# Kernel optimization log

Measured on AMD Instinct MI355X. Metric: run time of the kernel, lower is better.

The kernel has to match this reference:

```python
import jax, jax.numpy as jnp
import numpy as np

B, S, HID, NH, HD, NL = 2, 4096, 1024, 16, 64, 128
N_ITER = 6


def setup_inputs() -> dict:
    key = jax.random.key(0)
    ks = jax.random.split(key, 9)
    s = 0.02
    D = NH * HD
    return {
        "X": jax.random.normal(ks[0], (B, S, HID), jnp.float32),
        "mask": jnp.ones((B, S), jnp.float32),
        "Wq": jax.random.normal(ks[1], (HID, D), jnp.float32) * s,
        "bq": jnp.zeros((D,), jnp.float32),
        "Wk": jax.random.normal(ks[2], (HID, D), jnp.float32) * s,
        "bk": jnp.zeros((D,), jnp.float32),
        "Wv": jax.random.normal(ks[3], (HID, D), jnp.float32) * s,
        "bv": jnp.zeros((D,), jnp.float32),
        "Wo": jax.random.normal(ks[4], (D, HID), jnp.float32) * s,
        "bo": jnp.zeros((HID,), jnp.float32),
    }


def iterative_inv(mat, n_iter=N_ITER):
    # Newton-Schulz style pseudo-inverse iteration (Nystromformer 'original' init)
    I = jnp.eye(mat.shape[-1], dtype=mat.dtype)
    K = mat
    V = K.swapaxes(-1, -2) / jnp.max(jnp.sum(K, axis=-2))
    for _ in range(n_iter):
        KV = K @ V
        V = 0.25 * V @ (13.0 * I - KV @ (15.0 * I - KV @ (7.0 * I - KV)))
    return V


def nystrom_core(Q, K, V, mask):
    # Q,K,V: [B,NH,S,HD], mask: [B,S]
    scale = 1.0 / np.sqrt(np.sqrt(HD))  # 1/d^(1/4) applied to both Q and K
    m = mask[:, None, :, None]
    Q = Q * m * scale
    K = K * m * scale
    seg = S // NL
    # landmarks: mean over contiguous segments -> [B,NH,NL,HD]
    Ql = Q.reshape(B, NH, NL, seg, HD).mean(axis=-2)
    Kl = K.reshape(B, NH, NL, seg, HD).mean(axis=-2)
    k1 = jax.nn.softmax(jnp.einsum('bhsd,bhld->bhsl', Q, Kl), axis=-1)   # [B,NH,S,NL]
    k2 = jax.nn.softmax(jnp.einsum('bhld,bhmd->bhlm', Ql, Kl), axis=-1)  # [B,NH,NL,NL]
    k3 = jax.nn.softmax(
        jnp.einsum('bhld,bhsd->bhls', Ql, K) - 1e9 * (1.0 - mask[:, None, None, :]),
        axis=-1)                                                          # [B,NH,NL,S]
    return k1 @ iterative_inv(k2) @ (k3 @ V)                              # [B,NH,S,HD]


def reference(X, mask, Wq, bq, Wk, bk, Wv, bv, Wo, bo):
    def split(Y):  # [B,S,NH*HD] -> [B,NH,S,HD]
        return Y.reshape(B, S, NH, HD).transpose(0, 2, 1, 3)
    Q = split(X @ Wq + bq)
    K = split(X @ Wk + bk)
    V = split(X @ Wv + bv)
    attn = nystrom_core(Q.astype(jnp.float32), K.astype(jnp.float32),
                        V.astype(jnp.float32), mask.astype(jnp.float32))
    out = attn.transpose(0, 2, 1, 3).reshape(B, S, NH * HD)
    return out @ Wo + bo
```

## Files before the change

kernel.cpp:

```cpp
#include <hip/hip_runtime.h>
#include <math.h>

constexpr int cB = 2, cS = 4096, cHID = 1024, cNH = 16, cHD = 64, cNL = 128, cSEG = 32, cD = 1024, cBH = 32;
constexpr float cSCALE = 0.35355339059327373f;

typedef _Float16 f16x8 __attribute__((ext_vector_type(8)));
typedef float f32x4 __attribute__((ext_vector_type(4)));

__device__ inline void gload_lds16(const void* g, void* l) {
    __builtin_amdgcn_global_load_lds(
        (const __attribute__((address_space(1))) void*)g,
        (__attribute__((address_space(3))) void*)l, 16, 0, 0);
}

__global__ __launch_bounds__(256) void cast_x(const float* __restrict__ X, _Float16* __restrict__ Xh)
{
    int i = (blockIdx.x * 256 + threadIdx.x) * 4;
    float4 v = *reinterpret_cast<const float4*>(X + i);
    union { _Float16 h[4]; ushort4 u; } p;
    p.h[0] = (_Float16)v.x; p.h[1] = (_Float16)v.y; p.h[2] = (_Float16)v.z; p.h[3] = (_Float16)v.w;
    *reinterpret_cast<ushort4*>(Xh + i) = p.u;
}

__global__ __launch_bounds__(256) void wcast_t(
    const float* __restrict__ Wq, const float* __restrict__ Wk,
    const float* __restrict__ Wv, const float* __restrict__ Wo,
    _Float16* __restrict__ WqT, _Float16* __restrict__ WkT,
    _Float16* __restrict__ WvT, _Float16* __restrict__ WoT)
{
    __shared__ float tile[32][33];
    const int wsel = blockIdx.z;
    const float* W = (wsel == 0) ? Wq : (wsel == 1 ? Wk : (wsel == 2 ? Wv : Wo));
    _Float16* WT   = (wsel == 0) ? WqT : (wsel == 1 ? WkT : (wsel == 2 ? WvT : WoT));
    const int n0 = blockIdx.x * 32, k0 = blockIdx.y * 32;
    const int t = threadIdx.x;
    const int r = t >> 3, c = (t & 7) * 4;
    float4 v = *reinterpret_cast<const float4*>(W + (size_t)(k0 + r) * cD + n0 + c);
    tile[r][c] = v.x; tile[r][c + 1] = v.y; tile[r][c + 2] = v.z; tile[r][c + 3] = v.w;
    __syncthreads();
    union { _Float16 h[4]; ushort4 u; } p;
    p.h[0] = (_Float16)tile[c + 0][r]; p.h[1] = (_Float16)tile[c + 1][r];
    p.h[2] = (_Float16)tile[c + 2][r]; p.h[3] = (_Float16)tile[c + 3][r];
    *reinterpret_cast<ushort4*>(WT + (size_t)(n0 + r) * cHID + k0 + c) = p.u;
}

__global__ __launch_bounds__(256) void xm_kernel(
    const float* __restrict__ X, const float* __restrict__ mask,
    float* __restrict__ Xm, float* __restrict__ mbar)
{
    const int bl = blockIdx.x;
    const int b = bl >> 7, l = bl & 127;
    const int c = threadIdx.x * 4;
    float4 a = {0.f, 0.f, 0.f, 0.f};
    float msum = 0.f;
    for (int j = 0; j < cSEG; ++j) {
        float m = mask[b * cS + l * cSEG + j];
        float4 x = *reinterpret_cast<const float4*>(X + ((size_t)(b * cS + l * cSEG + j)) * cHID + c);
        a.x += m * x.x; a.y += m * x.y; a.z += m * x.z; a.w += m * x.w;
        msum += m;
    }
    const float inv = 1.0f / cSEG;
    a.x *= inv; a.y *= inv; a.z *= inv; a.w *= inv;
    *reinterpret_cast<float4*>(Xm + (size_t)bl * cHID + c) = a;
    if (threadIdx.x == 0) mbar[bl] = msum * inv;
}

__global__ __launch_bounds__(256) void qkv_gemm_f16(
    const _Float16* __restrict__ Xh, const float* __restrict__ mask,
    const _Float16* __restrict__ WqT, const _Float16* __restrict__ WkT, const _Float16* __restrict__ WvT,
    const float* __restrict__ bq, const float* __restrict__ bk, const float* __restrict__ bv,
    _Float16* __restrict__ Qh, _Float16* __restrict__ Kh, _Float16* __restrict__ Vh)
{
    __shared__ __align__(16) _Float16 As[128 * 64];
    __shared__ __align__(16) _Float16 Bs[128 * 64];
    const int wsel = blockIdx.z;
    const _Float16* WT = (wsel == 0) ? WqT : (wsel == 1 ? WkT : WvT);
    const float* bias  = (wsel == 0) ? bq  : (wsel == 1 ? bk  : bv);
    _Float16* Y        = (wsel == 0) ? Qh  : (wsel == 1 ? Kh  : Vh);
    const int n0 = blockIdx.x * 128, m0 = blockIdx.y * 128;
    const int t = threadIdx.x;
    const int wave = t >> 6, lane = t & 63;
    const int wm = (wave >> 1) * 64, wn = (wave & 1) * 64;
    const int quad = lane >> 4, l15 = lane & 15;
    const int srow = wave * 8 + (lane >> 3);
    const int scol = (lane & 7) * 8;

    f32x4 acc[4][4];
#pragma unroll
    for (int i = 0; i < 4; ++i)
#pragma unroll
        for (int j = 0; j < 4; ++j) acc[i][j] = (f32x4){0.f, 0.f, 0.f, 0.f};

    for (int k0 = 0; k0 < cHID; k0 += 64) {
        const _Float16* aSrc = Xh + (size_t)(m0 + srow) * cHID + k0 + scol;
        const _Float16* bSrc = WT + (size_t)(n0 + srow) * cHID + k0 + scol;
#pragma unroll
        for (int i = 0; i < 4; ++i) {
            gload_lds16(aSrc + (size_t)(i * 32) * cHID, &As[(wave * 8 + i * 32) * 64]);
            gload_lds16(bSrc + (size_t)(i * 32) * cHID, &Bs[(wave * 8 + i * 32) * 64]);
        }
        __syncthreads();
        f16x8 af[2][4], bf[2][4];
#pragma unroll
        for (int kh = 0; kh < 2; ++kh) {
#pragma unroll
            for (int mt = 0; mt < 4; ++mt)
                af[kh][mt] = *reinterpret_cast<const f16x8*>(&As[(wm + mt * 16 + l15) * 64 + kh * 32 + quad * 8]);
#pragma unroll
            for (int nt = 0; nt < 4; ++nt)
                bf[kh][nt] = *reinterpret_cast<const f16x8*>(&Bs[(wn + nt * 16 + l15) * 64 + kh * 32 + quad * 8]);
        }
#pragma unroll
        for (int kh = 0; kh < 2; ++kh)
#pragma unroll
            for (int mt = 0; mt < 4; ++mt)
#pragma unroll
                for (int nt = 0; nt < 4; ++nt)
                    acc[mt][nt] = __builtin_amdgcn_mfma_f32_16x16x32_f16(af[kh][mt], bf[kh][nt], acc[mt][nt], 0, 0, 0);
        __syncthreads();
    }
#pragma unroll
    for (int mt = 0; mt < 4; ++mt) {
#pragma unroll
        for (int r = 0; r < 4; ++r) {
            int R = m0 + wm + mt * 16 + quad * 4 + r;
            int b = R >> 12, s = R & (cS - 1);
            float msc = (wsel < 2) ? mask[b * cS + s] * cSCALE : 1.0f;
#pragma unroll
            for (int nt = 0; nt < 4; ++nt) {
                int Cc = n0 + wn + nt * 16 + l15;
                int h = Cc >> 6, d = Cc & 63;
                float val = (acc[mt][nt][r] + bias[Cc]) * msc;
                Y[((size_t)(b * cNH + h) * cS + s) * cHD + d] = (_Float16)val;
            }
        }
    }
}

__global__ __launch_bounds__(256) void out_gemm_f16(
    const _Float16* __restrict__ Ah, const _Float16* __restrict__ WT,
    const float* __restrict__ bias, float* __restrict__ Y)
{
    __shared__ __align__(16) _Float16 As[128 * 64];
    __shared__ __align__(16) _Float16 Bs[128 * 64];
    const int n0 = blockIdx.x * 128, m0 = blockIdx.y * 128;
    const int t = threadIdx.x;
    const int wave = t >> 6, lane = t & 63;
    const int wm = (wave >> 1) * 64, wn = (wave & 1) * 64;
    const int quad = lane >> 4, l15 = lane & 15;
    const int srow = wave * 8 + (lane >> 3);
    const int scol = (lane & 7) * 8;

    f32x4 acc[4][4];
#pragma unroll
    for (int i = 0; i < 4; ++i)
#pragma unroll
        for (int j = 0; j < 4; ++j) acc[i][j] = (f32x4){0.f, 0.f, 0.f, 0.f};

    for (int k0 = 0; k0 < cD; k0 += 64) {
        const _Float16* aSrc = Ah + (size_t)(m0 + srow) * cD + k0 + scol;
        const _Float16* bSrc = WT + (size_t)(n0 + srow) * cD + k0 + scol;
#pragma unroll
        for (int i = 0; i < 4; ++i) {
            gload_lds16(aSrc + (size_t)(i * 32) * cD, &As[(wave * 8 + i * 32) * 64]);
            gload_lds16(bSrc + (size_t)(i * 32) * cD, &Bs[(wave * 8 + i * 32) * 64]);
        }
        __syncthreads();
        f16x8 af[2][4], bf[2][4];
#pragma unroll
        for (int kh = 0; kh < 2; ++kh) {
#pragma unroll
            for (int mt = 0; mt < 4; ++mt)
                af[kh][mt] = *reinterpret_cast<const f16x8*>(&As[(wm + mt * 16 + l15) * 64 + kh * 32 + quad * 8]);
#pragma unroll
            for (int nt = 0; nt < 4; ++nt)
                bf[kh][nt] = *reinterpret_cast<const f16x8*>(&Bs[(wn + nt * 16 + l15) * 64 + kh * 32 + quad * 8]);
        }
#pragma unroll
        for (int kh = 0; kh < 2; ++kh)
#pragma unroll
            for (int mt = 0; mt < 4; ++mt)
#pragma unroll
                for (int nt = 0; nt < 4; ++nt)
                    acc[mt][nt] = __builtin_amdgcn_mfma_f32_16x16x32_f16(af[kh][mt], bf[kh][nt], acc[mt][nt], 0, 0, 0);
        __syncthreads();
    }
#pragma unroll
    for (int mt = 0; mt < 4; ++mt) {
#pragma unroll
        for (int r = 0; r < 4; ++r) {
            int R = m0 + wm + mt * 16 + quad * 4 + r;
#pragma unroll
            for (int nt = 0; nt < 4; ++nt) {
                int Cc = n0 + wn + nt * 16 + l15;
                Y[(size_t)R * cHID + Cc] = acc[mt][nt][r] + bias[Cc];
            }
        }
    }
}

__global__ __launch_bounds__(256) void lgemm(
    const float* __restrict__ Xm, const float* __restrict__ mbar,
    const float* __restrict__ Wq, const float* __restrict__ bq,
    const float* __restrict__ Wk, const float* __restrict__ bk,
    float* __restrict__ Ql, float* __restrict__ Kl,
    _Float16* __restrict__ Qlh, _Float16* __restrict__ Klh)
{
    __shared__ __align__(16) float As[16][68];
    __shared__ __align__(16) float Bs[16][68];
    const int tid = threadIdx.x;
    const int wsel = blockIdx.z;
    const float* W    = wsel ? Wk : Wq;
    const float* bias = wsel ? bk : bq;
    float* Yl         = wsel ? Kl : Ql;
    _Float16* Ylh     = wsel ? Klh : Qlh;
    const int c0 = blockIdx.x * 64, r0 = blockIdx.y * 64;
    const int tx = tid & 15, ty = tid >> 4;
    const int am = tid >> 2, ak = (tid & 3) * 4;
    const int bkk = tid >> 4, bn = (tid & 15) * 4;

    float acc[4][4] = {};
    for (int k0 = 0; k0 < cHID; k0 += 16) {
        float4 a4 = *reinterpret_cast<const float4*>(Xm + (size_t)(r0 + am) * cHID + k0 + ak);
        As[ak + 0][am] = a4.x; As[ak + 1][am] = a4.y; As[ak + 2][am] = a4.z; As[ak + 3][am] = a4.w;
        float4 b4 = *reinterpret_cast<const float4*>(W + (size_t)(k0 + bkk) * cD + c0 + bn);
        *reinterpret_cast<float4*>(&Bs[bkk][bn]) = b4;
        __syncthreads();
#pragma unroll
        for (int kk = 0; kk < 16; ++kk) {
            float4 av  = *reinterpret_cast<const float4*>(&As[kk][ty * 4]);
            float4 bv4 = *reinterpret_cast<const float4*>(&Bs[kk][tx * 4]);
            float a_[4] = {av.x, av.y, av.z, av.w};
            float b_[4] = {bv4.x, bv4.y, bv4.z, bv4.w};
#pragma unroll
            for (int i = 0; i < 4; ++i)
#pragma unroll
                for (int j = 0; j < 4; ++j) acc[i][j] += a_[i] * b_[j];
        }
        __syncthreads();
    }
#pragma unroll
    for (int i = 0; i < 4; ++i) {
        int r = r0 + ty * 4 + i;
        int b = r >> 7, l = r & 127;
        float mb = mbar[r];
#pragma unroll
        for (int j = 0; j < 4; ++j) {
            int c = c0 + tx * 4 + j;
            int h = c >> 6, d = c & 63;
            float val = (acc[i][j] + mb * bias[c]) * cSCALE;
            size_t idx = ((size_t)(b * cNH + h) * cNL + l) * cHD + d;
            Yl[idx] = val;
            Ylh[idx] = (_Float16)val;
        }
    }
}

__global__ __launch_bounds__(128) void k2_softmax(
    const float* __restrict__ Ql, const float* __restrict__ Kl, float* __restrict__ k2)
{
    __shared__ __align__(16) float qrow[64];
    __shared__ float red[128];
    int bh = blockIdx.x >> 7, i = blockIdx.x & 127;
    int j = threadIdx.x;
    if (j < 64) qrow[j] = Ql[(bh * cNL + i) * cHD + j];
    __syncthreads();
    const float4* q4  = reinterpret_cast<const float4*>(qrow);
    const float4* kl4 = reinterpret_cast<const float4*>(Kl + (bh * cNL + j) * cHD);
    float dot = 0.f;
#pragma unroll
    for (int u = 0; u < 16; ++u) {
        float4 a = q4[u], b = kl4[u];
        dot += a.x * b.x + a.y * b.y + a.z * b.z + a.w * b.w;
    }
    red[j] = dot; __syncthreads();
    for (int off = 64; off > 0; off >>= 1) { if (j < off) red[j] = fmaxf(red[j], red[j + off]); __syncthreads(); }
    float m = red[0]; __syncthreads();
    float e = expf(dot - m);
    red[j] = e; __syncthreads();
    for (int off = 64; off > 0; off >>= 1) { if (j < off) red[j] += red[j + off]; __syncthreads(); }
    k2[(bh * cNL + i) * cNL + j] = e / red[0];
}

__global__ __launch_bounds__(128) void colsum_max(const float* __restrict__ k2, int* __restrict__ cmax)
{
    __shared__ float red[128];
    int bh = blockIdx.x, j = threadIdx.x;
    float s = 0.f;
    for (int i = 0; i < cNL; ++i) s += k2[(bh * cNL + i) * cNL + j];
    red[j] = s; __syncthreads();
    for (int off = 64; off > 0; off >>= 1) { if (j < off) red[j] = fmaxf(red[j], red[j + off]); __syncthreads(); }
    if (j == 0) atomicMax(cmax, __float_as_int(red[0]));
}

__device__ inline void split2(float v, _Float16& h, _Float16& l) {
    h = (_Float16)v;
    l = (_Float16)(v - (float)h);
}

#define NYS_MFMA(a, b, c) __builtin_amdgcn_mfma_f32_16x16x32_f16((a), (b), (c), 0, 0, 0)

#define NYS_PRODUCT(PH, PL, LH, LL)                                                     \
    {                                                                                   \
        _Pragma("unroll")                                                               \
        for (int nt_ = 0; nt_ < 8; ++nt_) {                                             \
            f32x4 a0_ = (f32x4){0.f, 0.f, 0.f, 0.f};                                    \
            f32x4 a1_ = (f32x4){0.f, 0.f, 0.f, 0.f};                                    \
            _Pragma("unroll")                                                           \
            for (int k0_ = 0; k0_ < 4; ++k0_) {                                         \
                f16x8 bh_ = *reinterpret_cast<const f16x8*>(&PH[(nt_ * 16 + l15) * 136 + k0_ * 32 + quad * 8]); \
                f16x8 bl_ = *reinterpret_cast<const f16x8*>(&PL[(nt_ * 16 + l15) * 136 + k0_ * 32 + quad * 8]); \
                a0_ = NYS_MFMA(LH[0][k0_], bh_, a0_);                                   \
                a1_ = NYS_MFMA(LH[1][k0_], bh_, a1_);                                   \
                a0_ = NYS_MFMA(LL[0][k0_], bh_, a0_);                                   \
                a1_ = NYS_MFMA(LL[1][k0_], bh_, a1_);                                   \
                a0_ = NYS_MFMA(LH[0][k0_], bl_, a0_);                                   \
                a1_ = NYS_MFMA(LH[1][k0_], bl_, a1_);                                   \
            }                                                                           \
            acc[0][nt_] = a0_; acc[1][nt_] = a1_;                                       \
        }                                                                               \
    }

#define NYS_SCATTER_W(alphav)                                                           \
    {                                                                                   \
        _Pragma("unroll")                                                               \
        for (int mt_ = 0; mt_ < 2; ++mt_) {                                             \
            _Pragma("unroll")                                                           \
            for (int nt_ = 0; nt_ < 8; ++nt_) {                                         \
                int col_ = nt_ * 16 + l15;                                              \
                int rb_  = wave * 32 + mt_ * 16 + quad * 4;                             \
                ushort4 ph_, pl_;                                                       \
                _Pragma("unroll")                                                       \
                for (int r_ = 0; r_ < 4; ++r_) {                                        \
                    float v_ = ((rb_ + r_) == col_ ? (alphav) : 0.f) - acc[mt_][nt_][r_]; \
                    _Float16 h_, l_; split2(v_, h_, l_);                                \
                    ((unsigned short*)&ph_)[r_] = __builtin_bit_cast(unsigned short, h_); \
                    ((unsigned short*)&pl_)[r_] = __builtin_bit_cast(unsigned short, l_); \
                }                                                                       \
                *reinterpret_cast<ushort4*>(&Whi_s[col_ * 136 + rb_]) = ph_;            \
                *reinterpret_cast<ushort4*>(&Wlo_s[col_ * 136 + rb_]) = pl_;            \
            }                                                                           \
        }                                                                               \
    }

__global__ __launch_bounds__(256, 1) void nys_fused(
    const float* __restrict__ k2, const int* __restrict__ cmax, float* __restrict__ V6)
{
    __shared__ __align__(16) _Float16 Vhi_s[128 * 136];
    __shared__ __align__(16) _Float16 Vlo_s[128 * 136];
    __shared__ __align__(16) _Float16 Whi_s[128 * 136];
    __shared__ __align__(16) _Float16 Wlo_s[128 * 136];
    const int bh = blockIdx.x;
    const int t = threadIdx.x;
    const int wave = t >> 6, lane = t & 63;
    const int quad = lane >> 4, l15 = lane & 15;
    const float* Kg = k2 + (size_t)bh * (cNL * cNL);
    const float invc = 1.0f / __int_as_float(*cmax);

#pragma unroll
    for (int i = 0; i < 16; ++i) {
        int idx = t + i * 256;
        int row = idx >> 5, c4 = (idx & 31) * 4;
        float4 v = *reinterpret_cast<const float4*>(Kg + (size_t)row * cNL + c4);
        ushort4 ph, pl;
        _Float16 h, l;
        split2(v.x * invc, h, l); ((unsigned short*)&ph)[0] = __builtin_bit_cast(unsigned short, h); ((unsigned short*)&pl)[0] = __builtin_bit_cast(unsigned short, l);
        split2(v.y * invc, h, l); ((unsigned short*)&ph)[1] = __builtin_bit_cast(unsigned short, h); ((unsigned short*)&pl)[1] = __builtin_bit_cast(unsigned short, l);
        split2(v.z * invc, h, l); ((unsigned short*)&ph)[2] = __builtin_bit_cast(unsigned short, h); ((unsigned short*)&pl)[2] = __builtin_bit_cast(unsigned short, l);
        split2(v.w * invc, h, l); ((unsigned short*)&ph)[3] = __builtin_bit_cast(unsigned short, h); ((unsigned short*)&pl)[3] = __builtin_bit_cast(unsigned short, l);
        *reinterpret_cast<ushort4*>(&Vhi_s[row * 136 + c4]) = ph;
        *reinterpret_cast<ushort4*>(&Vlo_s[row * 136 + c4]) = pl;
    }

    f16x8 Khi[2][4], Klo[2][4];
#pragma unroll
    for (int mt = 0; mt < 2; ++mt) {
        const int rowL = wave * 32 + mt * 16 + l15;
#pragma unroll
        for (int k0 = 0; k0 < 4; ++k0) {
            const float* src = Kg + (size_t)rowL * cNL + k0 * 32 + quad * 8;
            union { f16x8 v; _Float16 e[8]; } hh, ll;
#pragma unroll
            for (int j = 0; j < 8; ++j) split2(src[j], hh.e[j], ll.e[j]);
            Khi[mt][k0] = hh.v; Klo[mt][k0] = ll.v;
        }
    }
    __syncthreads();

    f32x4 acc[2][8];
    f16x8 Ahi[2][4], Alo[2][4];

    for (int it = 0; it < 6; ++it) {
        NYS_PRODUCT(Vhi_s, Vlo_s, Khi, Klo);
        NYS_SCATTER_W(7.0f);
        __syncthreads();

#pragma unroll
        for (int mt = 0; mt < 2; ++mt) {
            const int rowL = wave * 32 + mt * 16 + l15;
#pragma unroll
            for (int k0 = 0; k0 < 4; ++k0) {
                union { f16x8 v; _Float16 e[8]; } hh, ll;
#pragma unroll
                for (int j = 0; j < 8; ++j) {
                    int kk = k0 * 32 + quad * 8 + j;
                    float s = (float)Whi_s[kk * 136 + rowL] + (float)Wlo_s[kk * 136 + rowL];
                    float a = ((kk == rowL) ? 7.0f : 0.0f) - s;
                    split2(a, hh.e[j], ll.e[j]);
                }
                Ahi[mt][k0] = hh.v; Alo[mt][k0] = ll.v;
            }
        }

        NYS_PRODUCT(Whi_s, Wlo_s, Ahi, Alo);
        __syncthreads();
        NYS_SCATTER_W(15.0f);
        __syncthreads();

        NYS_PRODUCT(Whi_s, Wlo_s, Ahi, Alo);

        f16x8 Vlh[2][4], Vll[2][4];
#pragma unroll
        for (int mt = 0; mt < 2; ++mt) {
            const int rowL = wave * 32 + mt * 16 + l15;
#pragma unroll
            for (int k0 = 0; k0 < 4; ++k0) {
                union { f16x8 v; _Float16 e[8]; } hh, ll;
#pragma unroll
                for (int j = 0; j < 8; ++j) {
                    int kk = k0 * 32 + quad * 8 + j;
                    hh.e[j] = Vhi_s[kk * 136 + rowL];
                    ll.e[j] = Vlo_s[kk * 136 + rowL];
                }
                Vlh[mt][k0] = hh.v; Vll[mt][k0] = ll.v;
            }
        }
        __syncthreads();
        NYS_SCATTER_W(13.0f);
        __syncthreads();

        NYS_PRODUCT(Whi_s, Wlo_s, Vlh, Vll);
        if (it < 5) {
#pragma unroll
            for (int mt = 0; mt < 2; ++mt) {
#pragma unroll
                for (int nt = 0; nt < 8; ++nt) {
                    int col = nt * 16 + l15;
                    int rb  = wave * 32 + mt * 16 + quad * 4;
                    ushort4 ph, pl;
#pragma unroll
                    for (int r = 0; r < 4; ++r) {
                        _Float16 h, l; split2(0.25f * acc[mt][nt][r], h, l);
                        ((unsigned short*)&ph)[r] = __builtin_bit_cast(unsigned short, h);
                        ((unsigned short*)&pl)[r] = __builtin_bit_cast(unsigned short, l);
                    }
                    *reinterpret_cast<ushort4*>(&Vhi_s[col * 136 + rb]) = ph;
                    *reinterpret_cast<ushort4*>(&Vlo_s[col * 136 + rb]) = pl;
                }
            }
            __syncthreads();
        }
    }
#pragma unroll
    for (int mt = 0; mt < 2; ++mt)
#pragma unroll
        for (int nt = 0; nt < 8; ++nt)
#pragma unroll
            for (int r = 0; r < 4; ++r) {
                int row = wave * 32 + mt * 16 + quad * 4 + r;
                int col = nt * 16 + l15;
                V6[(size_t)bh * (cNL * cNL) + row * cNL + col] = 0.25f * acc[mt][nt][r];
            }
}

__global__ __launch_bounds__(256) void vtrans(const _Float16* __restrict__ Vh, _Float16* __restrict__ VTh)
{
    __shared__ ushort T[64][72];
    const int s0 = blockIdx.x * 64, bh = blockIdx.y;
    const int t = threadIdx.x;
    const _Float16* vb = Vh + ((size_t)bh * cS + s0) * cHD;
#pragma unroll
    for (int i = 0; i < 2; ++i) {
        int idx = t + i * 256;
        int row = idx >> 3, c8 = idx & 7;
        f16x8 v = *reinterpret_cast<const f16x8*>(vb + (size_t)row * cHD + c8 * 8);
#pragma unroll
        for (int j = 0; j < 8; ++j) T[row][c8 * 8 + j] = ((ushort*)&v)[j];
    }
    __syncthreads();
    _Float16* vt = VTh + (size_t)bh * cHD * cS;
#pragma unroll
    for (int i = 0; i < 2; ++i) {
        int idx = t + i * 256;
        int d = idx >> 3, s8 = idx & 7;
        f16x8 o;
#pragma unroll
        for (int j = 0; j < 8; ++j) ((ushort*)&o)[j] = T[s8 * 8 + j][d];
        *reinterpret_cast<f16x8*>(vt + (size_t)d * cS + s0 + s8 * 8) = o;
    }
}

__global__ __launch_bounds__(256) void k3v_mfma(
    const _Float16* __restrict__ Qlh, const _Float16* __restrict__ Kh,
    const _Float16* __restrict__ VTh, const float* __restrict__ mask,
    float* __restrict__ Opart, float* __restrict__ mpart, float* __restrict__ spart)
{
    __shared__ __align__(16) _Float16 Ps[128 * 72];
    __shared__ float msk[256];
    const int z = blockIdx.x, bh = blockIdx.y;
    const int b = bh >> 4;
    const int sbase = z * 256;
    const int t = threadIdx.x;
    const int wave = t >> 6, lane = t & 63;
    const int quad = lane >> 4, l15 = lane & 15;

    msk[t] = mask[b * cS + sbase + t];

    f16x8 aq[2][2];
    const _Float16* qlg = Qlh + (size_t)bh * cNL * cHD;
#pragma unroll
    for (int mt = 0; mt < 2; ++mt)
#pragma unroll
        for (int k0 = 0; k0 < 2; ++k0)
            aq[mt][k0] = *reinterpret_cast<const f16x8*>(
                qlg + (size_t)(wave * 32 + mt * 16 + l15) * cHD + k0 * 32 + quad * 8);

    float mrun[2][4], srun[2][4];
    f32x4 accO[2][4];
#pragma unroll
    for (int mt = 0; mt < 2; ++mt)
#pragma unroll
        for (int r = 0; r < 4; ++r) { mrun[mt][r] = -1e30f; srun[mt][r] = 0.f; }
#pragma unroll
    for (int mt = 0; mt < 2; ++mt)
#pragma unroll
        for (int dt = 0; dt < 4; ++dt) accO[mt][dt] = (f32x4){0.f, 0.f, 0.f, 0.f};

    __syncthreads();

    const _Float16* kg = Kh + (size_t)bh * cS * cHD;
    const _Float16* vg = VTh + (size_t)bh * cHD * cS;

    for (int step = 0; step < 4; ++step) {
        const int st = sbase + step * 64;
        f32x4 accS[2][4];
#pragma unroll
        for (int mt = 0; mt < 2; ++mt)
#pragma unroll
            for (int nt = 0; nt < 4; ++nt) accS[mt][nt] = (f32x4){0.f, 0.f, 0.f, 0.f};
#pragma unroll
        for (int k0 = 0; k0 < 2; ++k0)
#pragma unroll
            for (int nt = 0; nt < 4; ++nt) {
                f16x8 bk = *reinterpret_cast<const f16x8*>(
                    kg + (size_t)(st + nt * 16 + l15) * cHD + k0 * 32 + quad * 8);
#pragma unroll
                for (int mt = 0; mt < 2; ++mt)
                    accS[mt][nt] = __builtin_amdgcn_mfma_f32_16x16x32_f16(aq[mt][k0], bk, accS[mt][nt], 0, 0, 0);
            }
#pragma unroll
        for (int nt = 0; nt < 4; ++nt) {
            float pen = 1e9f * (1.0f - msk[step * 64 + nt * 16 + l15]);
#pragma unroll
            for (int mt = 0; mt < 2; ++mt)
#pragma unroll
                for (int r = 0; r < 4; ++r) accS[mt][nt][r] -= pen;
        }
#pragma unroll
        for (int mt = 0; mt < 2; ++mt) {
#pragma unroll
            for (int r = 0; r < 4; ++r) {
                float tmax = fmaxf(fmaxf(accS[mt][0][r], accS[mt][1][r]),
                                   fmaxf(accS[mt][2][r], accS[mt][3][r]));
#pragma unroll
                for (int w = 1; w < 16; w <<= 1) tmax = fmaxf(tmax, __shfl_xor(tmax, w, 16));
                float mnew = fmaxf(mrun[mt][r], tmax);
                float alpha = __expf(mrun[mt][r] - mnew);
                float ts = 0.f;
#pragma unroll
                for (int nt = 0; nt < 4; ++nt) {
                    float e = __expf(accS[mt][nt][r] - mnew);
                    accS[mt][nt][r] = e; ts += e;
                }
#pragma unroll
                for (int w = 1; w < 16; w <<= 1) ts += __shfl_xor(ts, w, 16);
                srun[mt][r] = srun[mt][r] * alpha + ts;
                mrun[mt][r] = mnew;
#pragma unroll
                for (int dt = 0; dt < 4; ++dt) accO[mt][dt][r] *= alpha;
            }
        }
#pragma unroll
        for (int mt = 0; mt < 2; ++mt)
#pragma unroll
            for (int nt = 0; nt < 4; ++nt)
#pragma unroll
                for (int r = 0; r < 4; ++r)
                    Ps[(wave * 32 + mt * 16 + quad * 4 + r) * 72 + nt * 16 + l15] =
                        (_Float16)accS[mt][nt][r];
#pragma unroll
        for (int k0 = 0; k0 < 2; ++k0) {
            f16x8 ap[2];
#pragma unroll
            for (int mt = 0; mt < 2; ++mt)
                ap[mt] = *reinterpret_cast<const f16x8*>(
                    &Ps[(wave * 32 + mt * 16 + l15) * 72 + k0 * 32 + quad * 8]);
#pragma unroll
            for (int dt = 0; dt < 4; ++dt) {
                f16x8 bv = *reinterpret_cast<const f16x8*>(
                    vg + (size_t)(dt * 16 + l15) * cS + st + k0 * 32 + quad * 8);
#pragma unroll
                for (int mt = 0; mt < 2; ++mt)
                    accO[mt][dt] = __builtin_amdgcn_mfma_f32_16x16x32_f16(ap[mt], bv, accO[mt][dt], 0, 0, 0);
            }
        }
    }
    const int rowbase = bh * cNL + wave * 32;
#pragma unroll
    for (int mt = 0; mt < 2; ++mt)
#pragma unroll
        for (int dt = 0; dt < 4; ++dt)
#pragma unroll
            for (int r = 0; r < 4; ++r)
                Opart[(size_t)(z * 4096 + rowbase + mt * 16 + quad * 4 + r) * cHD + dt * 16 + l15] =
                    accO[mt][dt][r];
    if (l15 == 0) {
#pragma unroll
        for (int mt = 0; mt < 2; ++mt)
#pragma unroll
            for (int r = 0; r < 4; ++r) {
                int prow = z * 4096 + rowbase + mt * 16 + quad * 4 + r;
                mpart[prow] = mrun[mt][r];
                spart[prow] = srun[mt][r];
            }
    }
}

__global__ __launch_bounds__(256) void k3v_reduce(
    const float* __restrict__ Opart, const float* __restrict__ mpart,
    const float* __restrict__ spart, float* __restrict__ CV)
{
    const int t = threadIdx.x;
    const int row = blockIdx.x * 4 + (t >> 6);
    const int d = t & 63;
    float mstar = -1e30f;
#pragma unroll
    for (int z = 0; z < 16; ++z) mstar = fmaxf(mstar, mpart[z * 4096 + row]);
    float ssum = 0.f, acc = 0.f;
#pragma unroll
    for (int z = 0; z < 16; ++z) {
        float w = __expf(mpart[z * 4096 + row] - mstar);
        ssum += w * spart[z * 4096 + row];
        acc  += w * Opart[(size_t)(z * 4096 + row) * cHD + d];
    }
    CV[(size_t)row * cHD + d] = acc / ssum;
}

__global__ __launch_bounds__(256) void w2_matmul(
    const float* __restrict__ V6, const float* __restrict__ CV, _Float16* __restrict__ W2T)
{
    __shared__ __align__(16) float CVs[128][64];
    const int bh = blockIdx.x, t = threadIdx.x;
    for (int k = 0; k < 32; ++k) { int idx = t + k * 256; CVs[idx >> 6][idx & 63] = CV[bh * 8192 + idx]; }
    __syncthreads();
    const int tx = t & 15, ty = t >> 4;
    float acc[8][4] = {};
    for (int k = 0; k < 128; ++k) {
        float4 b4 = *reinterpret_cast<const float4*>(&CVs[k][tx * 4]);
#pragma unroll
        for (int i = 0; i < 8; ++i) {
            float a = V6[(bh * cNL + ty * 8 + i) * cNL + k];
            acc[i][0] += a * b4.x; acc[i][1] += a * b4.y; acc[i][2] += a * b4.z; acc[i][3] += a * b4.w;
        }
    }
    _Float16* wt = W2T + (size_t)bh * cHD * cNL;
#pragma unroll
    for (int i = 0; i < 8; ++i)
#pragma unroll
        for (int j = 0; j < 4; ++j)
            wt[(size_t)(tx * 4 + j) * cNL + ty * 8 + i] = (_Float16)acc[i][j];
}

__global__ __launch_bounds__(256) void k1_mfma(
    const _Float16* __restrict__ Qh, const _Float16* __restrict__ Klh,
    const _Float16* __restrict__ W2T, _Float16* __restrict__ ctxh)
{
    __shared__ __align__(16) _Float16 Qs[64 * 72];
    __shared__ __align__(16) _Float16 Ps[64 * 136];
    const int s0 = blockIdx.x * 64, bh = blockIdx.y;
    const int b = bh >> 4, h = bh & 15;
    const int t = threadIdx.x;
    const int wave = t >> 6, lane = t & 63;
    const int quad = lane >> 4, l15 = lane & 15;

    {
        const _Float16* qg = Qh + ((size_t)bh * cS + s0) * cHD;
#pragma unroll
        for (int i = 0; i < 2; ++i) {
            int idx = t + i * 256;
            int row = idx >> 3, c8 = idx & 7;
            *reinterpret_cast<f16x8*>(&Qs[row * 72 + c8 * 8]) =
                *reinterpret_cast<const f16x8*>(qg + (size_t)row * cHD + c8 * 8);
        }
    }
    __syncthreads();

    const _Float16* klg = Klh + (size_t)bh * cNL * cHD;
    f32x4 accS[8];
#pragma unroll
    for (int nt = 0; nt < 8; ++nt) accS[nt] = (f32x4){0.f, 0.f, 0.f, 0.f};
#pragma unroll
    for (int k0 = 0; k0 < 2; ++k0) {
        f16x8 aq = *reinterpret_cast<const f16x8*>(&Qs[(wave * 16 + l15) * 72 + k0 * 32 + quad * 8]);
#pragma unroll
        for (int nt = 0; nt < 8; ++nt) {
            f16x8 bk = *reinterpret_cast<const f16x8*>(klg + (size_t)(nt * 16 + l15) * cHD + k0 * 32 + quad * 8);
            accS[nt] = __builtin_amdgcn_mfma_f32_16x16x32_f16(aq, bk, accS[nt], 0, 0, 0);
        }
    }

    float rmax[4] = {-1e30f, -1e30f, -1e30f, -1e30f};
#pragma unroll
    for (int nt = 0; nt < 8; ++nt)
#pragma unroll
        for (int r = 0; r < 4; ++r) rmax[r] = fmaxf(rmax[r], accS[nt][r]);
#pragma unroll
    for (int r = 0; r < 4; ++r)
#pragma unroll
        for (int w = 1; w < 16; w <<= 1) rmax[r] = fmaxf(rmax[r], __shfl_xor(rmax[r], w, 16));
    float rsum[4] = {0.f, 0.f, 0.f, 0.f};
#pragma unroll
    for (int nt = 0; nt < 8; ++nt)
#pragma unroll
        for (int r = 0; r < 4; ++r) { accS[nt][r] = __expf(accS[nt][r] - rmax[r]); rsum[r] += accS[nt][r]; }
#pragma unroll
    for (int r = 0; r < 4; ++r) {
#pragma unroll
        for (int w = 1; w < 16; w <<= 1) rsum[r] += __shfl_xor(rsum[r], w, 16);
        rsum[r] = 1.0f / rsum[r];
    }
#pragma unroll
    for (int nt = 0; nt < 8; ++nt)
#pragma unroll
        for (int r = 0; r < 4; ++r)
            Ps[(wave * 16 + quad * 4 + r) * 136 + nt * 16 + l15] = (_Float16)(accS[nt][r] * rsum[r]);
    __syncthreads();

    const _Float16* wtg = W2T + (size_t)bh * cHD * cNL;
    f32x4 accO[4];
#pragma unroll
    for (int nt = 0; nt < 4; ++nt) accO[nt] = (f32x4){0.f, 0.f, 0.f, 0.f};
#pragma unroll
    for (int k0 = 0; k0 < 4; ++k0) {
        f16x8 ap = *reinterpret_cast<const f16x8*>(&Ps[(wave * 16 + l15) * 136 + k0 * 32 + quad * 8]);
#pragma unroll
        for (int nt = 0; nt < 4; ++nt) {
            f16x8 bw = *reinterpret_cast<const f16x8*>(wtg + (size_t)(nt * 16 + l15) * cNL + k0 * 32 + quad * 8);
            accO[nt] = __builtin_amdgcn_mfma_f32_16x16x32_f16(ap, bw, accO[nt], 0, 0, 0);
        }
    }
#pragma unroll
    for (int nt = 0; nt < 4; ++nt)
#pragma unroll
        for (int r = 0; r < 4; ++r) {
            int s = s0 + wave * 16 + quad * 4 + r;
            int d = nt * 16 + l15;
            ctxh[((size_t)(b * cS) + s) * cD + h * cHD + d] = (_Float16)accO[nt][r];
        }
}

extern "C" void kernel_launch(void* const* d_in, const int* in_sizes, int n_in,
                              void* d_out, int out_size, void* d_ws, size_t ws_size,
                              hipStream_t stream)
{
    const float* X    = (const float*)d_in[0];
    const float* mask = (const float*)d_in[1];
    const float* Wq   = (const float*)d_in[2];
    const float* bq   = (const float*)d_in[3];
    const float* Wk   = (const float*)d_in[4];
    const float* bk   = (const float*)d_in[5];
    const float* Wv   = (const float*)d_in[6];
    const float* bv   = (const float*)d_in[7];
    const float* Wo   = (const float*)d_in[8];
    const float* bo   = (const float*)d_in[9];
    float* out = (float*)d_out;

    float* ws = (float*)d_ws;
    size_t off = 0;
    const size_t szQKV = (size_t)cBH * cS * cHD;
    const size_t szL   = (size_t)cBH * cNL * cHD;
    const size_t szM   = (size_t)cBH * cNL * cNL;
    float* Qr   = ws + off; off += szQKV;
    float* Kr   = ws + off; off += szQKV;
    float* Vr   = ws + off; off += szQKV;
    _Float16* Xh  = (_Float16*)(ws + off); off += szQKV / 2;
    _Float16* WqT = (_Float16*)(ws + off); off += 524288;
    _Float16* WkT = (_Float16*)(ws + off); off += 524288;
    _Float16* WvT = (_Float16*)(ws + off); off += 524288;
    _Float16* WoT = (_Float16*)(ws + off); off += 524288;
    float* Xm   = ws + off; off += (size_t)cB * cNL * cHID;
    float* mbar = ws + off; off += 256;
    float* Ql  = ws + off; off += szL;
    float* Kl  = ws + off; off += szL;
    float* k2  = ws + off; off += szM;
    float* Vb0 = ws + off; off += szM;
    float* Vb1 = ws + off; off += szM;
    float* Zb  = ws + off; off += szM;
    float* T2b = ws + off; off += szM;
    float* T3b = ws + off; off += szM;
    float* CV  = ws + off; off += szL;
    _Float16* Qlh  = (_Float16*)(ws + off); off += szL / 2;
    _Float16* Klh  = (_Float16*)(ws + off); off += szL / 2;
    _Float16* W2Th = (_Float16*)(ws + off); off += szL / 2;
    int*   cmax = (int*)(ws + off); off += 16;
    float* mpart = ws + off; off += 65536;
    float* spart = ws + off; off += 65536;

    _Float16* Qh   = (_Float16*)Qr;
    float*    Opart = Qr + szQKV / 2;
    _Float16* Kh   = (_Float16*)Kr;
    _Float16* ctxh = (_Float16*)(Kr + szQKV / 2);
    _Float16* Vh   = (_Float16*)Vr;
    _Float16* VTh  = (_Float16*)(Vr + szQKV / 2);

    (void)Vb1; (void)Zb; (void)T2b; (void)T3b;

    hipMemsetAsync(cmax, 0, sizeof(int), stream);

    cast_x<<<(int)(szQKV / 1024), 256, 0, stream>>>(X, Xh);
    wcast_t<<<dim3(32, 32, 4), 256, 0, stream>>>(Wq, Wk, Wv, Wo, WqT, WkT, WvT, WoT);
    xm_kernel<<<cB * cNL, 256, 0, stream>>>(X, mask, Xm, mbar);

    qkv_gemm_f16<<<dim3(cD / 128, (cB * cS) / 128, 3), 256, 0, stream>>>(
        Xh, mask, WqT, WkT, WvT, bq, bk, bv, Qh, Kh, Vh);
    vtrans<<<dim3(cS / 64, cBH), 256, 0, stream>>>(Vh, VTh);
    lgemm<<<dim3(cD / 64, (cB * cNL) / 64, 2), 256, 0, stream>>>(Xm, mbar, Wq, bq, Wk, bk, Ql, Kl, Qlh, Klh);

    k2_softmax<<<cBH * cNL, 128, 0, stream>>>(Ql, Kl, k2);
    colsum_max<<<cBH, 128, 0, stream>>>(k2, cmax);

    nys_fused<<<cBH, 256, 0, stream>>>(k2, cmax, Vb0);

    k3v_mfma<<<dim3(16, cBH), 256, 0, stream>>>(Qlh, Kh, VTh, mask, Opart, mpart, spart);
    k3v_reduce<<<1024, 256, 0, stream>>>(Opart, mpart, spart, CV);
    w2_matmul<<<cBH, 256, 0, stream>>>(Vb0, CV, W2Th);
    k1_mfma<<<dim3(cS / 64, cBH), 256, 0, stream>>>(Qh, Klh, W2Th, ctxh);
    out_gemm_f16<<<dim3(cHID / 128, (cB * cS) / 128), 256, 0, stream>>>(ctxh, WoT, bo, out);
}
```

Before: 556.1 us.

## Split Nystrom inverse kernel across 8 waves with 2D wave tiling

The fused Newton-Schulz inverse kernel now runs 512 threads per block instead of 256. Waves are arranged as a 4x2 grid, so each wave computes a 32x64 output tile instead of 32x128, which halves its accumulator registers. The final product now loads the V operand per k-slice instead of staging all of it in registers first, and initial loads use float4. This is meant to add latency hiding to a kernel that runs only 32 blocks, at the cost of an extra barrier per iteration.

```diff
diff --git a/kernel.cpp b/kernel.cpp
--- a/kernel.cpp
+++ b/kernel.cpp
@@ -303,13 +303,14 @@
 #define NYS_PRODUCT(PH, PL, LH, LL)                                                     \
     {                                                                                   \
         _Pragma("unroll")                                                               \
-        for (int nt_ = 0; nt_ < 8; ++nt_) {                                             \
+        for (int nt_ = 0; nt_ < 4; ++nt_) {                                             \
             f32x4 a0_ = (f32x4){0.f, 0.f, 0.f, 0.f};                                    \
             f32x4 a1_ = (f32x4){0.f, 0.f, 0.f, 0.f};                                    \
             _Pragma("unroll")                                                           \
             for (int k0_ = 0; k0_ < 4; ++k0_) {                                         \
-                f16x8 bh_ = *reinterpret_cast<const f16x8*>(&PH[(nt_ * 16 + l15) * 136 + k0_ * 32 + quad * 8]); \
-                f16x8 bl_ = *reinterpret_cast<const f16x8*>(&PL[(nt_ * 16 + l15) * 136 + k0_ * 32 + quad * 8]); \
+                const int boff_ = (wcb + nt_ * 16) * 136 + k0_ * 32 + quad * 8;         \
+                f16x8 bh_ = *reinterpret_cast<const f16x8*>(&PH[boff_]);                \
+                f16x8 bl_ = *reinterpret_cast<const f16x8*>(&PL[boff_]);                \
                 a0_ = NYS_MFMA(LH[0][k0_], bh_, a0_);                                   \
                 a1_ = NYS_MFMA(LH[1][k0_], bh_, a1_);                                   \
                 a0_ = NYS_MFMA(LL[0][k0_], bh_, a0_);                                   \
@@ -326,9 +327,9 @@
         _Pragma("unroll")                                                               \
         for (int mt_ = 0; mt_ < 2; ++mt_) {                                             \
             _Pragma("unroll")                                                           \
-            for (int nt_ = 0; nt_ < 8; ++nt_) {                                         \
-                int col_ = nt_ * 16 + l15;                                              \
-                int rb_  = wave * 32 + mt_ * 16 + quad * 4;                             \
+            for (int nt_ = 0; nt_ < 4; ++nt_) {                                         \
+                int col_ = wcb + nt_ * 16;                                              \
+                int rb_  = wr * 32 + mt_ * 16 + quad * 4;                               \
                 ushort4 ph_, pl_;                                                       \
                 _Pragma("unroll")                                                       \
                 for (int r_ = 0; r_ < 4; ++r_) {                                        \
@@ -343,7 +344,7 @@
         }                                                                               \
     }
 
-__global__ __launch_bounds__(256, 1) void nys_fused(
+__global__ __launch_bounds__(512, 2) void nys_fused(
     const float* __restrict__ k2, const int* __restrict__ cmax, float* __restrict__ V6)
 {
     __shared__ __align__(16) _Float16 Vhi_s[128 * 136];
@@ -353,13 +354,15 @@
     const int bh = blockIdx.x;
     const int t = threadIdx.x;
     const int wave = t >> 6, lane = t & 63;
+    const int wr = wave >> 1, wc = wave & 1;
     const int quad = lane >> 4, l15 = lane & 15;
+    const int wcb = wc * 64 + l15;
     const float* Kg = k2 + (size_t)bh * (cNL * cNL);
     const float invc = 1.0f / __int_as_float(*cmax);
 
 #pragma unroll
-    for (int i = 0; i < 16; ++i) {
-        int idx = t + i * 256;
+    for (int i = 0; i < 8; ++i) {
+        int idx = t + i * 512;
         int row = idx >> 5, c4 = (idx & 31) * 4;
         float4 v = *reinterpret_cast<const float4*>(Kg + (size_t)row * cNL + c4);
         ushort4 ph, pl;
@@ -375,19 +378,23 @@
     f16x8 Khi[2][4], Klo[2][4];
 #pragma unroll
     for (int mt = 0; mt < 2; ++mt) {
-        const int rowL = wave * 32 + mt * 16 + l15;
+        const int rowL = wr * 32 + mt * 16 + l15;
 #pragma unroll
         for (int k0 = 0; k0 < 4; ++k0) {
             const float* src = Kg + (size_t)rowL * cNL + k0 * 32 + quad * 8;
+            float4 v0 = *reinterpret_cast<const float4*>(src);
+            float4 v1 = *reinterpret_cast<const float4*>(src + 4);
             union { f16x8 v; _Float16 e[8]; } hh, ll;
-#pragma unroll
-            for (int j = 0; j < 8; ++j) split2(src[j], hh.e[j], ll.e[j]);
+            split2(v0.x, hh.e[0], ll.e[0]); split2(v0.y, hh.e[1], ll.e[1]);
+            split2(v0.z, hh.e[2], ll.e[2]); split2(v0.w, hh.e[3], ll.e[3]);
+            split2(v1.x, hh.e[4], ll.e[4]); split2(v1.y, hh.e[5], ll.e[5]);
+            split2(v1.z, hh.e[6], ll.e[6]); split2(v1.w, hh.e[7], ll.e[7]);
             Khi[mt][k0] = hh.v; Klo[mt][k0] = ll.v;
         }
     }
     __syncthreads();
 
-    f32x4 acc[2][8];
+    f32x4 acc[2][4];
     f16x8 Ahi[2][4], Alo[2][4];
 
     for (int it = 0; it < 6; ++it) {
@@ -397,7 +404,7 @@
 
 #pragma unroll
         for (int mt = 0; mt < 2; ++mt) {
-            const int rowL = wave * 32 + mt * 16 + l15;
+            const int rowL = wr * 32 + mt * 16 + l15;
 #pragma unroll
             for (int k0 = 0; k0 < 4; ++k0) {
                 union { f16x8 v; _Float16 e[8]; } hh, ll;
@@ -418,13 +425,20 @@
         __syncthreads();
 
         NYS_PRODUCT(Whi_s, Wlo_s, Ahi, Alo);
-
-        f16x8 Vlh[2][4], Vll[2][4];
-#pragma unroll
-        for (int mt = 0; mt < 2; ++mt) {
-            const int rowL = wave * 32 + mt * 16 + l15;
-#pragma unroll
-            for (int k0 = 0; k0 < 4; ++k0) {
+        __syncthreads();
+        NYS_SCATTER_W(13.0f);
+        __syncthreads();
+
+#pragma unroll
+        for (int mt = 0; mt < 2; ++mt)
+#pragma unroll
+            for (int nt = 0; nt < 4; ++nt) acc[mt][nt] = (f32x4){0.f, 0.f, 0.f, 0.f};
+#pragma unroll
+        for (int k0 = 0; k0 < 4; ++k0) {
+            f16x8 Vlh[2], Vll[2];
+#pragma unroll
+            for (int mt = 0; mt < 2; ++mt) {
+                const int rowL = wr * 32 + mt * 16 + l15;
                 union { f16x8 v; _Float16 e[8]; } hh, ll;
 #pragma unroll
                 for (int j = 0; j < 8; ++j) {
@@ -432,21 +446,29 @@
                     hh.e[j] = Vhi_s[kk * 136 + rowL];
                     ll.e[j] = Vlo_s[kk * 136 + rowL];
                 }
-                Vlh[mt][k0] = hh.v; Vll[mt][k0] = ll.v;
-            }
-        }
-        __syncthreads();
-        NYS_SCATTER_W(13.0f);
-        __syncthreads();
-
-        NYS_PRODUCT(Whi_s, Wlo_s, Vlh, Vll);
+                Vlh[mt] = hh.v; Vll[mt] = ll.v;
+            }
+#pragma unroll
+            for (int nt = 0; nt < 4; ++nt) {
+                const int boff = (wcb + nt * 16) * 136 + k0 * 32 + quad * 8;
+                f16x8 bh_ = *reinterpret_cast<const f16x8*>(&Whi_s[boff]);
+                f16x8 bl_ = *reinterpret_cast<const f16x8*>(&Wlo_s[boff]);
+                acc[0][nt] = NYS_MFMA(Vlh[0], bh_, acc[0][nt]);
+                acc[1][nt] = NYS_MFMA(Vlh[1], bh_, acc[1][nt]);
+                acc[0][nt] = NYS_MFMA(Vll[0], bh_, acc[0][nt]);
+                acc[1][nt] = NYS_MFMA(Vll[1], bh_, acc[1][nt]);
+                acc[0][nt] = NYS_MFMA(Vlh[0], bl_, acc[0][nt]);
+                acc[1][nt] = NYS_MFMA(Vlh[1], bl_, acc[1][nt]);
+            }
+        }
         if (it < 5) {
+            __syncthreads();
 #pragma unroll
             for (int mt = 0; mt < 2; ++mt) {
 #pragma unroll
-                for (int nt = 0; nt < 8; ++nt) {
-                    int col = nt * 16 + l15;
-                    int rb  = wave * 32 + mt * 16 + quad * 4;
+                for (int nt = 0; nt < 4; ++nt) {
+                    int col = wcb + nt * 16;
+                    int rb  = wr * 32 + mt * 16 + quad * 4;
                     ushort4 ph, pl;
 #pragma unroll
                     for (int r = 0; r < 4; ++r) {
@@ -464,11 +486,11 @@
 #pragma unroll
     for (int mt = 0; mt < 2; ++mt)
 #pragma unroll
-        for (int nt = 0; nt < 8; ++nt)
+        for (int nt = 0; nt < 4; ++nt)
 #pragma unroll
             for (int r = 0; r < 4; ++r) {
-                int row = wave * 32 + mt * 16 + quad * 4 + r;
-                int col = nt * 16 + l15;
+                int row = wr * 32 + mt * 16 + quad * 4 + r;
+                int col = wcb + nt * 16;
                 V6[(size_t)bh * (cNL * cNL) + row * cNL + col] = 0.25f * acc[mt][nt][r];
             }
 }
@@ -839,7 +861,7 @@
     k2_softmax<<<cBH * cNL, 128, 0, stream>>>(Ql, Kl, k2);
     colsum_max<<<cBH, 128, 0, stream>>>(k2, cmax);
 
-    nys_fused<<<cBH, 256, 0, stream>>>(k2, cmax, Vb0);
+    nys_fused<<<cBH, 512, 0, stream>>>(k2, cmax, Vb0);
 
     k3v_mfma<<<dim3(16, cBH), 256, 0, stream>>>(Qlh, Kh, VTh, mask, Opart, mpart, spart);
     k3v_reduce<<<1024, 256, 0, stream>>>(Opart, mpart, spart, CV);
```

After: 544.3 us. 1.02x faster.
